# Optimization experiments

Hardware: AMD Instinct MI355X
Metric: run time of the kernel (lower is better)

The kernel has to match this reference:

```python
import jax, jax.numpy as jnp
import numpy as np

N, D, E, T = 30000, 256, 300000, 2
HID, OUT, HEADS = 64, 256, 8


def setup_inputs() -> dict:
    key = jax.random.key(0)
    ks = jax.random.split(key, 16)
    g = lambda k, shape, fan_in: jax.random.normal(k, shape, jnp.float32) / np.sqrt(fan_in)
    inp = {
        'x': jax.random.normal(ks[0], (N, D), jnp.float32),
        'edge_index': jax.random.randint(ks[1], (T, 2, E), 0, N, jnp.int32),
        'w1_l': g(ks[2], (T, D, HEADS * HID), D),
        'b1_l': jnp.zeros((T, HEADS * HID), jnp.float32),
        'w1_r': g(ks[3], (T, D, HEADS * HID), D),
        'b1_r': jnp.zeros((T, HEADS * HID), jnp.float32),
        'att1': g(ks[4], (T, HEADS, HID), HID),
        'bias1': jnp.zeros((T, HEADS * HID), jnp.float32),
        'w2_l': g(ks[5], (T, HEADS * HID, OUT), HEADS * HID),
        'b2_l': jnp.zeros((T, OUT), jnp.float32),
        'w2_r': g(ks[6], (T, HEADS * HID, OUT), HEADS * HID),
        'b2_r': jnp.zeros((T, OUT), jnp.float32),
        'att2': g(ks[7], (T, 1, OUT), OUT),
        'bias2': jnp.zeros((T, OUT), jnp.float32),
        'w_lin': g(ks[8], (OUT, OUT), OUT),
        'b_lin': jnp.zeros((OUT,), jnp.float32),
    }
    return inp


def _gatv2(x, src, dst, w_l, b_l, w_r, b_r, att, bias, num_nodes):
    # GATv2Conv: e = att . leaky_relu(W_l x_src + W_r x_dst); softmax over in-edges of dst;
    # out = scatter_add(alpha * W_l x_src) per destination; concat heads + bias.
    H, C = att.shape
    xl = (x @ w_l + b_l).reshape(num_nodes, H, C)
    xr = (x @ w_r + b_r).reshape(num_nodes, H, C)
    h = jax.nn.leaky_relu(xl[src] + xr[dst], 0.2)      # [E, H, C]
    e = jnp.einsum('ehc,hc->eh', h, att)               # [E, H]
    m = jax.ops.segment_max(e, dst, num_segments=num_nodes)
    p = jnp.exp(e - m[dst])
    s = jax.ops.segment_sum(p, dst, num_segments=num_nodes)
    alpha = p / s[dst]                                 # softmax over neighbors
    out = jax.ops.segment_sum(xl[src] * alpha[:, :, None], dst, num_segments=num_nodes)
    return out.reshape(num_nodes, H * C) + bias


def reference(x, edge_index, w1_l, b1_l, w1_r, b1_r, att1, bias1,
              w2_l, b2_l, w2_r, b2_r, att2, bias2, w_lin, b_lin):
    n = x.shape[0]
    loop = jnp.arange(n, dtype=edge_index.dtype)  # GATv2Conv default add_self_loops=True
    srcs, dsts = [], []
    for t in range(edge_index.shape[0]):
        srcs.append(jnp.concatenate([edge_index[t, 0], loop]))
        dsts.append(jnp.concatenate([edge_index[t, 1], loop]))

    # conv1 (heads=8, concat) with HeteroConv aggr='sum'
    h1 = jnp.zeros((n, w1_l.shape[2]), x.dtype)
    for t in range(len(srcs)):
        h1 = h1 + _gatv2(x, srcs[t], dsts[t], w1_l[t], b1_l[t], w1_r[t], b1_r[t], att1[t], bias1[t], n)
    h1 = jax.nn.elu(h1)

    # conv2 (heads=1, concat=False -> mean over 1 head == identity)
    h2 = jnp.zeros((n, w2_l.shape[2]), x.dtype)
    for t in range(len(srcs)):
        h2 = h2 + _gatv2(h1, srcs[t], dsts[t], w2_l[t], b2_l[t], w2_r[t], b2_r[t], att2[t], bias2[t], n)
    h2 = jax.nn.elu(h2)

    return h2 @ w_lin + b_lin
```

## Files before the change

kernel.cpp:

```cpp
#include <hip/hip_runtime.h>
#include <math.h>

#define N_NODES 30000
#define D_IN    256
#define E_EDGES 300000
#define T_TYPES 2
#define HEADS   8
#define HID     64
#define F1      512
#define OUT_F   256
#define EP      (E_EDGES + N_NODES)

typedef __attribute__((ext_vector_type(8))) short bf16x8;
typedef __attribute__((ext_vector_type(4))) float f32x4;

__device__ __forceinline__ unsigned short f2bf(float f) {
    unsigned u = __float_as_uint(f);
    unsigned r = 0x7fffu + ((u >> 16) & 1u);
    return (unsigned short)((u + r) >> 16);
}
__device__ __forceinline__ float bf2f(unsigned short h) {
    return __uint_as_float(((unsigned)h) << 16);
}

__device__ __forceinline__ void gload16(const void* g, void* l) {
    __builtin_amdgcn_global_load_lds(
        (const __attribute__((address_space(1))) unsigned int*)g,
        (__attribute__((address_space(3))) unsigned int*)l, 16, 0, 0);
}

#define PREP_W1   (8 * 65536)
#define PREP_W2   (4 * 131072)
#define PREP_WL   65536
#define PREP_CNT  (T_TYPES * N_NODES)
#define PREP_TOT  (PREP_W1 + PREP_W2 + PREP_WL + PREP_CNT)

__global__ void prep_kernel(const float* __restrict__ w1_l, const float* __restrict__ w1_r,
                            const float* __restrict__ w2_l, const float* __restrict__ w2_r,
                            const float* __restrict__ w_lin,
                            unsigned short* __restrict__ wt1h, unsigned short* __restrict__ wt1l,
                            unsigned short* __restrict__ wt2h, unsigned short* __restrict__ wt2l,
                            unsigned short* __restrict__ wtLh, unsigned short* __restrict__ wtLl,
                            int* __restrict__ count) {
    int idx = blockIdx.x * blockDim.x + threadIdx.x;
    if (idx < PREP_W1) {
        int n = idx & 255, k = (idx >> 8) & 255, mat = idx >> 16;
        int h = mat & 1, lr = (mat >> 1) & 1, t = mat >> 2;
        const float* src = lr ? w1_r : w1_l;
        float v = src[(size_t)t * 256 * 512 + (size_t)k * 512 + h * 256 + n];
        unsigned short hi = f2bf(v);
        unsigned short lo = f2bf(v - bf2f(hi));
        size_t o = (size_t)mat * 65536 + (size_t)n * 256 + k;
        wt1h[o] = hi; wt1l[o] = lo;
        return;
    }
    idx -= PREP_W1;
    if (idx < PREP_W2) {
        int n = idx & 255, k = (idx >> 8) & 511, mat = idx >> 17;
        int lr = mat & 1, t = mat >> 1;
        const float* src = lr ? w2_r : w2_l;
        float v = src[(size_t)t * 512 * 256 + (size_t)k * 256 + n];
        unsigned short hi = f2bf(v);
        unsigned short lo = f2bf(v - bf2f(hi));
        size_t o = (size_t)mat * 131072 + (size_t)n * 512 + k;
        wt2h[o] = hi; wt2l[o] = lo;
        return;
    }
    idx -= PREP_W2;
    if (idx < PREP_WL) {
        int n = idx & 255, k = idx >> 8;
        float v = w_lin[k * 256 + n];
        unsigned short hi = f2bf(v);
        unsigned short lo = f2bf(v - bf2f(hi));
        size_t o = (size_t)n * 256 + k;
        wtLh[o] = hi; wtLl[o] = lo;
        return;
    }
    idx -= PREP_WL;
    if (idx < PREP_CNT) count[idx] = 0;
}

__global__ void hist_kernel(const int* __restrict__ ei, int* __restrict__ count) {
    int idx = blockIdx.x * blockDim.x + threadIdx.x;
    if (idx >= T_TYPES * EP) return;
    int t = idx / EP, i = idx - t * EP;
    int dst = (i < E_EDGES) ? ei[t * 2 * E_EDGES + E_EDGES + i] : (i - E_EDGES);
    atomicAdd(&count[t * N_NODES + dst], 1);
}

#define SCAN_NB 30

__global__ __launch_bounds__(256) void scan_bsum_kernel(const int* __restrict__ cnt,
                                                        int* __restrict__ bsum) {
    int t = blockIdx.y, b = blockIdx.x;
    const int* c = cnt + t * N_NODES;
    int i0 = b * 1024 + threadIdx.x * 4;
    int s = 0;
    #pragma unroll
    for (int j = 0; j < 4; ++j) { int i = i0 + j; if (i < N_NODES) s += c[i]; }
    #pragma unroll
    for (int m = 1; m < 64; m <<= 1) s += __shfl_xor(s, m);
    __shared__ int wsum[4];
    int l = threadIdx.x & 63, w = threadIdx.x >> 6;
    if (l == 0) wsum[w] = s;
    __syncthreads();
    if (threadIdx.x == 0) bsum[t * SCAN_NB + b] = wsum[0] + wsum[1] + wsum[2] + wsum[3];
}

__global__ void scan_base_kernel(int* __restrict__ bsum) {
    int t = threadIdx.x;
    if (t >= T_TYPES) return;
    int acc = 0;
    for (int b = 0; b < SCAN_NB; ++b) {
        int v = bsum[t * SCAN_NB + b];
        bsum[t * SCAN_NB + b] = acc;
        acc += v;
    }
}

__global__ __launch_bounds__(256) void scan_write_kernel(int* __restrict__ cnt,
                                                         const int* __restrict__ bsum,
                                                         int* __restrict__ off) {
    int t = blockIdx.y, b = blockIdx.x;
    int tid = threadIdx.x;
    int* c = cnt + t * N_NODES;
    int* o = off + t * (N_NODES + 1);
    int i0 = b * 1024 + tid * 4;
    int v[4]; int s = 0;
    #pragma unroll
    for (int j = 0; j < 4; ++j) { int i = i0 + j; v[j] = (i < N_NODES) ? c[i] : 0; s += v[j]; }
    __shared__ int ps[256];
    ps[tid] = s;
    __syncthreads();
    for (int ofs = 1; ofs < 256; ofs <<= 1) {
        int x = (tid >= ofs) ? ps[tid - ofs] : 0;
        __syncthreads();
        ps[tid] += x;
        __syncthreads();
    }
    int base = bsum[t * SCAN_NB + b] + ps[tid] - s;
    #pragma unroll
    for (int j = 0; j < 4; ++j) {
        int i = i0 + j;
        if (i < N_NODES) { o[i] = base; base += v[j]; c[i] = 0; }
    }
    if (b == 0 && tid == 0) o[N_NODES] = EP;
}

__global__ void scatter_kernel(const int* __restrict__ ei, const int* __restrict__ offsets,
                               int* __restrict__ cursor, int* __restrict__ csr_src) {
    int idx = blockIdx.x * blockDim.x + threadIdx.x;
    if (idx >= T_TYPES * EP) return;
    int t = idx / EP, i = idx - t * EP;
    int src, dst;
    if (i < E_EDGES) {
        src = ei[t * 2 * E_EDGES + i];
        dst = ei[t * 2 * E_EDGES + E_EDGES + i];
    } else {
        src = dst = i - E_EDGES;
    }
    int pos = offsets[t * (N_NODES + 1) + dst] + atomicAdd(&cursor[t * N_NODES + dst], 1);
    csr_src[t * EP + pos] = src;
}

template <int ASPLIT>
__global__ __launch_bounds__(256) void gemm_mfma_kernel(
        const void* __restrict__ A0v, const void* __restrict__ A1v, int lda,
        const unsigned short* __restrict__ Bh0, const unsigned short* __restrict__ Bl0,
        const float* __restrict__ bias0, float* __restrict__ C0,
        const unsigned short* __restrict__ Bh1, const unsigned short* __restrict__ Bl1,
        const float* __restrict__ bias1, float* __restrict__ C1,
        int M, int K) {
    const unsigned short* Bh = blockIdx.y ? Bh1 : Bh0;
    const unsigned short* Bl = blockIdx.y ? Bl1 : Bl0;
    const float* bias = blockIdx.y ? bias1 : bias0;
    float* C = blockIdx.y ? C1 : C0;
    const float* Af          = (const float*)A0v;
    const unsigned short* Ah = (const unsigned short*)A0v;
    const unsigned short* Al = (const unsigned short*)A1v;

    __shared__ unsigned short Ah_s[64 * 32], Al_s[64 * 32];
    __shared__ unsigned short Bh_s[256 * 32], Bl_s[256 * 32];
    int t = threadIdx.x;
    int row0 = blockIdx.x * 64;
    int w = t >> 6;
    int l = t & 63;
    int fm = l & 15;
    int fg = l >> 4;

    f32x4 acc[4][4];
    const f32x4 zf = {0.f, 0.f, 0.f, 0.f};
    #pragma unroll
    for (int i = 0; i < 4; ++i)
        #pragma unroll
        for (int j = 0; j < 4; ++j) acc[i][j] = zf;

    int ar = t >> 3, af = t & 7;
    int rs = l >> 2, cs = l & 3;

    for (int k0 = 0; k0 < K; k0 += 32) {
        #pragma unroll
        for (int g = 0; g < 4; ++g) {
            int n = g * 64 + w * 16 + rs;
            int swn = (n >> 1) & 3;
            size_t so = (size_t)n * K + k0 + ((cs ^ swn) * 8);
            gload16(&Bh[so], &Bh_s[(g * 64 + w * 16) * 32]);
            gload16(&Bl[so], &Bl_s[(g * 64 + w * 16) * 32]);
        }
        if constexpr (ASPLIT == 0) {
            #pragma unroll
            for (int v = 0; v < 2; ++v) {
                int r = v * 32 + ar;
                int rg = row0 + r;
                float4 a4 = make_float4(0.f, 0.f, 0.f, 0.f);
                if (rg < M) a4 = *(const float4*)&Af[(size_t)rg * lda + k0 + af * 4];
                ushort4 hi, lo;
                hi.x = f2bf(a4.x); lo.x = f2bf(a4.x - bf2f(hi.x));
                hi.y = f2bf(a4.y); lo.y = f2bf(a4.y - bf2f(hi.y));
                hi.z = f2bf(a4.z); lo.z = f2bf(a4.z - bf2f(hi.z));
                hi.w = f2bf(a4.w); lo.w = f2bf(a4.w - bf2f(hi.w));
                int ke = (af * 4) ^ (((r >> 1) & 3) << 3);
                *(ushort4*)&Ah_s[r * 32 + ke] = hi;
                *(ushort4*)&Al_s[r * 32 + ke] = lo;
            }
        } else {
            int r = w * 16 + rs;
            int rg = row0 + r;
            if (rg >= M) rg = M - 1;
            int swn = (r >> 1) & 3;
            size_t so = (size_t)rg * lda + k0 + ((cs ^ swn) * 8);
            gload16(&Ah[so], &Ah_s[(w * 16) * 32]);
            gload16(&Al[so], &Al_s[(w * 16) * 32]);
        }
        __syncthreads();
        bf16x8 ahf[4], alf[4], bhf[4], blf[4];
        #pragma unroll
        for (int i = 0; i < 4; ++i) {
            int r = i * 16 + fm;
            int ke = (fg * 8) ^ (((r >> 1) & 3) << 3);
            ahf[i] = *(const bf16x8*)&Ah_s[r * 32 + ke];
            alf[i] = *(const bf16x8*)&Al_s[r * 32 + ke];
        }
        #pragma unroll
        for (int j = 0; j < 4; ++j) {
            int n = w * 64 + j * 16 + fm;
            int ke = (fg * 8) ^ (((n >> 1) & 3) << 3);
            bhf[j] = *(const bf16x8*)&Bh_s[n * 32 + ke];
            blf[j] = *(const bf16x8*)&Bl_s[n * 32 + ke];
        }
        #pragma unroll
        for (int i = 0; i < 4; ++i)
            #pragma unroll
            for (int j = 0; j < 4; ++j) {
                acc[i][j] = __builtin_amdgcn_mfma_f32_16x16x32_bf16(ahf[i], bhf[j], acc[i][j], 0, 0, 0);
                acc[i][j] = __builtin_amdgcn_mfma_f32_16x16x32_bf16(ahf[i], blf[j], acc[i][j], 0, 0, 0);
                acc[i][j] = __builtin_amdgcn_mfma_f32_16x16x32_bf16(alf[i], bhf[j], acc[i][j], 0, 0, 0);
            }
        __syncthreads();
    }
    #pragma unroll
    for (int j = 0; j < 4; ++j) {
        int col = w * 64 + j * 16 + fm;
        float bv = bias[col];
        #pragma unroll
        for (int i = 0; i < 4; ++i) {
            #pragma unroll
            for (int q = 0; q < 4; ++q) {
                int rg = row0 + i * 16 + fg * 4 + q;
                if (rg < M) C[(size_t)rg * 256 + col] = acc[i][j][q] + bv;
            }
        }
    }
}

template <int RW, int MODE>
__global__ __launch_bounds__(256) void gat_edge_kernel(
        const float* __restrict__ xl, const float* __restrict__ xr,
        const float* __restrict__ att,
        const int* __restrict__ offs, const int* __restrict__ csr,
        float* __restrict__ out, int ldo,
        const float* __restrict__ eb0, const float* __restrict__ eb1,
        unsigned short* __restrict__ sh, unsigned short* __restrict__ sl) {
    int wave = (blockIdx.x * blockDim.x + threadIdx.x) >> 6;
    int lane = threadIdx.x & 63;
    if (wave >= N_NODES) return;
    int d = wave;
    int q4 = lane * 4;
    float attr[4], xrr[4];
    *(float4*)&attr[0] = *(const float4*)&att[q4];
    *(float4*)&xrr[0]  = *(const float4*)&xr[(size_t)d * 256 + q4];
    float m = -INFINITY, s = 0.f;
    float acc[4] = {0.f, 0.f, 0.f, 0.f};
    int p0 = offs[d], p1 = offs[d + 1];
    int p = p0;
    for (; p + 2 <= p1; p += 2) {
        int s0 = csr[p], s1 = csr[p + 1];
        float xv0[4], xv1[4];
        *(float4*)&xv0[0] = *(const float4*)&xl[(size_t)s0 * 256 + q4];
        *(float4*)&xv1[0] = *(const float4*)&xl[(size_t)s1 * 256 + q4];
        float e0 = 0.f, e1 = 0.f;
        #pragma unroll
        for (int q = 0; q < 4; ++q) {
            float h0 = xv0[q] + xrr[q];
            float h1 = xv1[q] + xrr[q];
            h0 = (h0 > 0.f) ? h0 : 0.2f * h0;
            h1 = (h1 > 0.f) ? h1 : 0.2f * h1;
            e0 += attr[q] * h0;
            e1 += attr[q] * h1;
        }
        #pragma unroll
        for (int msk = 1; msk < RW; msk <<= 1) {
            e0 += __shfl_xor(e0, msk);
            e1 += __shfl_xor(e1, msk);
        }
        float mn = fmaxf(m, e0);
        float sc = __expf(m - mn);
        float pe = __expf(e0 - mn);
        s = s * sc + pe;
        #pragma unroll
        for (int q = 0; q < 4; ++q) acc[q] = acc[q] * sc + pe * xv0[q];
        m = mn;
        mn = fmaxf(m, e1);
        sc = __expf(m - mn);
        pe = __expf(e1 - mn);
        s = s * sc + pe;
        #pragma unroll
        for (int q = 0; q < 4; ++q) acc[q] = acc[q] * sc + pe * xv1[q];
        m = mn;
    }
    if (p < p1) {
        int s0 = csr[p];
        float xv0[4];
        *(float4*)&xv0[0] = *(const float4*)&xl[(size_t)s0 * 256 + q4];
        float e0 = 0.f;
        #pragma unroll
        for (int q = 0; q < 4; ++q) {
            float h0 = xv0[q] + xrr[q];
            h0 = (h0 > 0.f) ? h0 : 0.2f * h0;
            e0 += attr[q] * h0;
        }
        #pragma unroll
        for (int msk = 1; msk < RW; msk <<= 1) e0 += __shfl_xor(e0, msk);
        float mn = fmaxf(m, e0);
        float sc = __expf(m - mn);
        float pe = __expf(e0 - mn);
        s = s * sc + pe;
        #pragma unroll
        for (int q = 0; q < 4; ++q) acc[q] = acc[q] * sc + pe * xv0[q];
        m = mn;
    }
    float inv = 1.f / s;
    float* dp = &out[(size_t)d * ldo + q4];
    if (MODE == 0) {
        *(float4*)dp = make_float4(acc[0] * inv, acc[1] * inv, acc[2] * inv, acc[3] * inv);
    } else if (MODE == 2) {
        #pragma unroll
        for (int q = 0; q < 4; ++q) {
            float v = dp[q] + acc[q] * inv + eb0[q4 + q] + eb1[q4 + q];
            dp[q] = (v > 0.f) ? v : (__expf(v) - 1.f);
        }
    } else {
        ushort4 hv, lv;
        float v0 = dp[0] + acc[0] * inv + eb0[q4 + 0] + eb1[q4 + 0];
        float v1 = dp[1] + acc[1] * inv + eb0[q4 + 1] + eb1[q4 + 1];
        float v2 = dp[2] + acc[2] * inv + eb0[q4 + 2] + eb1[q4 + 2];
        float v3 = dp[3] + acc[3] * inv + eb0[q4 + 3] + eb1[q4 + 3];
        v0 = (v0 > 0.f) ? v0 : (__expf(v0) - 1.f);
        v1 = (v1 > 0.f) ? v1 : (__expf(v1) - 1.f);
        v2 = (v2 > 0.f) ? v2 : (__expf(v2) - 1.f);
        v3 = (v3 > 0.f) ? v3 : (__expf(v3) - 1.f);
        hv.x = f2bf(v0); lv.x = f2bf(v0 - bf2f(hv.x));
        hv.y = f2bf(v1); lv.y = f2bf(v1 - bf2f(hv.y));
        hv.z = f2bf(v2); lv.z = f2bf(v2 - bf2f(hv.z));
        hv.w = f2bf(v3); lv.w = f2bf(v3 - bf2f(hv.w));
        *(ushort4*)&sh[(size_t)d * ldo + q4] = hv;
        *(ushort4*)&sl[(size_t)d * ldo + q4] = lv;
    }
}

extern "C" void kernel_launch(void* const* d_in, const int* in_sizes, int n_in,
                              void* d_out, int out_size, void* d_ws, size_t ws_size,
                              hipStream_t stream) {
    const float* x      = (const float*)d_in[0];
    const int*   ei     = (const int*)d_in[1];
    const float* w1_l   = (const float*)d_in[2];
    const float* b1_l   = (const float*)d_in[3];
    const float* w1_r   = (const float*)d_in[4];
    const float* b1_r   = (const float*)d_in[5];
    const float* att1   = (const float*)d_in[6];
    const float* bias1  = (const float*)d_in[7];
    const float* w2_l   = (const float*)d_in[8];
    const float* b2_l   = (const float*)d_in[9];
    const float* w2_r   = (const float*)d_in[10];
    const float* b2_r   = (const float*)d_in[11];
    const float* att2   = (const float*)d_in[12];
    const float* bias2  = (const float*)d_in[13];
    const float* w_lin  = (const float*)d_in[14];
    const float* b_lin  = (const float*)d_in[15];
    float* out = (float*)d_out;

    float* h1   = (float*)d_ws;
    float* bufA = h1 + (size_t)N_NODES * F1;
    float* bufB = bufA + (size_t)N_NODES * OUT_F;
    unsigned short* wt1h = (unsigned short*)(bufB + (size_t)N_NODES * OUT_F);
    unsigned short* wt1l = wt1h + 8 * 65536;
    unsigned short* wt2h = wt1l + 8 * 65536;
    unsigned short* wt2l = wt2h + 4 * 131072;
    unsigned short* wtLh = wt2l + 4 * 131072;
    unsigned short* wtLl = wtLh + 65536;
    int* count   = (int*)(wtLl + 65536);
    int* offsets = count + T_TYPES * N_NODES;
    int* bsum    = offsets + T_TYPES * (N_NODES + 1);
    int* csr     = bsum + T_TYPES * SCAN_NB;
    unsigned short* h2s_hi = (unsigned short*)h1;
    unsigned short* h2s_lo = h2s_hi + (size_t)N_NODES * OUT_F;

    prep_kernel<<<(PREP_TOT + 255) / 256, 256, 0, stream>>>(
        w1_l, w1_r, w2_l, w2_r, w_lin, wt1h, wt1l, wt2h, wt2l, wtLh, wtLl, count);

    int eblocks = (T_TYPES * EP + 255) / 256;
    hist_kernel<<<eblocks, 256, 0, stream>>>(ei, count);
    dim3 sgrid(SCAN_NB, T_TYPES);
    scan_bsum_kernel<<<sgrid, 256, 0, stream>>>(count, bsum);
    scan_base_kernel<<<1, 64, 0, stream>>>(bsum);
    scan_write_kernel<<<sgrid, 256, 0, stream>>>(count, bsum, offsets);
    scatter_kernel<<<eblocks, 256, 0, stream>>>(ei, offsets, count, csr);

    int gat_blocks = N_NODES / 4;
    dim3 ggrid((N_NODES + 63) / 64, 2);
    dim3 ggrid1((N_NODES + 63) / 64, 1);

    for (int t = 0; t < T_TYPES; ++t) {
        for (int hh = 0; hh < 2; ++hh) {
            int co = hh * 256;
            int ml = (t * 2 + 0) * 2 + hh, mr = (t * 2 + 1) * 2 + hh;
            gemm_mfma_kernel<0><<<ggrid, 256, 0, stream>>>(
                x, nullptr, D_IN,
                wt1h + (size_t)ml * 65536, wt1l + (size_t)ml * 65536, b1_l + t * F1 + co, bufA,
                wt1h + (size_t)mr * 65536, wt1l + (size_t)mr * 65536, b1_r + t * F1 + co, bufB,
                N_NODES, D_IN);
            if (t == 0)
                gat_edge_kernel<16, 0><<<gat_blocks, 256, 0, stream>>>(
                    bufA, bufB, att1 + t * F1 + co, offsets + t * (N_NODES + 1),
                    csr + (size_t)t * EP, h1 + co, F1, nullptr, nullptr, nullptr, nullptr);
            else
                gat_edge_kernel<16, 2><<<gat_blocks, 256, 0, stream>>>(
                    bufA, bufB, att1 + t * F1 + co, offsets + t * (N_NODES + 1),
                    csr + (size_t)t * EP, h1 + co, F1, bias1 + co, bias1 + F1 + co,
                    nullptr, nullptr);
        }
    }

    for (int t = 0; t < T_TYPES; ++t) {
        int ml = t * 2 + 0, mr = t * 2 + 1;
        gemm_mfma_kernel<0><<<ggrid, 256, 0, stream>>>(
            h1, nullptr, F1,
            wt2h + (size_t)ml * 131072, wt2l + (size_t)ml * 131072, b2_l + t * OUT_F, bufA,
            wt2h + (size_t)mr * 131072, wt2l + (size_t)mr * 131072, b2_r + t * OUT_F, bufB,
            N_NODES, F1);
        if (t == 0)
            gat_edge_kernel<64, 0><<<gat_blocks, 256, 0, stream>>>(
                bufA, bufB, att2 + t * OUT_F, offsets + t * (N_NODES + 1),
                csr + (size_t)t * EP, out, OUT_F, nullptr, nullptr, nullptr, nullptr);
        else
            gat_edge_kernel<64, 3><<<gat_blocks, 256, 0, stream>>>(
                bufA, bufB, att2 + t * OUT_F, offsets + t * (N_NODES + 1),
                csr + (size_t)t * EP, out, OUT_F, bias2, bias2 + OUT_F,
                h2s_hi, h2s_lo);
    }

    gemm_mfma_kernel<1><<<ggrid1, 256, 0, stream>>>(
        h2s_hi, h2s_lo, OUT_F,
        wtLh, wtLl, b_lin, out,
        wtLh, wtLl, b_lin, out,
        N_NODES, OUT_F);
}
```

Before: 892.3 us.

## Double-buffer shared-memory tiles in split-bf16 MFMA GEMM to overlap loads with compute

Shared-memory A and B tiles in the GEMM kernel are now double-buffered. The next K-slice is staged (async global-to-LDS loads for B and pre-split A, register prefetch for fp32 A) while MFMAs run on the current slice, so each iteration needs one barrier instead of two. The goal is to hide global load latency behind the matrix math. It doubles LDS use to about 80KB per block, which may cut occupancy, and fp32 A is held in registers one extra stage ahead.

```diff
diff --git a/kernel.cpp b/kernel.cpp
--- a/kernel.cpp
+++ b/kernel.cpp
@@ -163,6 +163,60 @@
     csr_src[t * EP + pos] = src;
 }
 
+#define STAGE_B(BUF, K0)                                                     \
+    do {                                                                     \
+        _Pragma("unroll")                                                    \
+        for (int g = 0; g < 4; ++g) {                                        \
+            int n_ = g * 64 + w * 16 + rs;                                   \
+            int swn_ = (n_ >> 1) & 3;                                        \
+            size_t so_ = (size_t)n_ * K + (K0) + ((cs ^ swn_) * 8);          \
+            gload16(&Bh[so_], &Bh_s[BUF][(g * 64 + w * 16) * 32]);           \
+            gload16(&Bl[so_], &Bl_s[BUF][(g * 64 + w * 16) * 32]);           \
+        }                                                                    \
+    } while (0)
+
+#define STAGE_A_DMA(BUF, K0)                                                 \
+    do {                                                                     \
+        int r_ = w * 16 + rs;                                                \
+        int rg_ = row0 + r_;                                                 \
+        if (rg_ >= M) rg_ = M - 1;                                           \
+        int swn_ = (r_ >> 1) & 3;                                            \
+        size_t so_ = (size_t)rg_ * lda + (K0) + ((cs ^ swn_) * 8);           \
+        gload16(&Ah[so_], &Ah_s[BUF][(w * 16) * 32]);                        \
+        gload16(&Al[so_], &Al_s[BUF][(w * 16) * 32]);                        \
+    } while (0)
+
+#define LOAD_A_REGS(K0)                                                      \
+    do {                                                                     \
+        int rg0_ = row0 + ar;                                                \
+        int rg1_ = row0 + 32 + ar;                                           \
+        aN0 = (rg0_ < M) ? *(const float4*)&Af[(size_t)rg0_ * lda + (K0) + af * 4] \
+                         : make_float4(0.f, 0.f, 0.f, 0.f);                  \
+        aN1 = (rg1_ < M) ? *(const float4*)&Af[(size_t)rg1_ * lda + (K0) + af * 4] \
+                         : make_float4(0.f, 0.f, 0.f, 0.f);                  \
+    } while (0)
+
+#define WRITE_A(BUF)                                                         \
+    do {                                                                     \
+        ushort4 hi_, lo_;                                                    \
+        int r_ = ar;                                                         \
+        hi_.x = f2bf(aN0.x); lo_.x = f2bf(aN0.x - bf2f(hi_.x));              \
+        hi_.y = f2bf(aN0.y); lo_.y = f2bf(aN0.y - bf2f(hi_.y));              \
+        hi_.z = f2bf(aN0.z); lo_.z = f2bf(aN0.z - bf2f(hi_.z));              \
+        hi_.w = f2bf(aN0.w); lo_.w = f2bf(aN0.w - bf2f(hi_.w));              \
+        int ke_ = (af * 4) ^ (((r_ >> 1) & 3) << 3);                         \
+        *(ushort4*)&Ah_s[BUF][r_ * 32 + ke_] = hi_;                          \
+        *(ushort4*)&Al_s[BUF][r_ * 32 + ke_] = lo_;                          \
+        r_ = 32 + ar;                                                        \
+        hi_.x = f2bf(aN1.x); lo_.x = f2bf(aN1.x - bf2f(hi_.x));              \
+        hi_.y = f2bf(aN1.y); lo_.y = f2bf(aN1.y - bf2f(hi_.y));              \
+        hi_.z = f2bf(aN1.z); lo_.z = f2bf(aN1.z - bf2f(hi_.z));              \
+        hi_.w = f2bf(aN1.w); lo_.w = f2bf(aN1.w - bf2f(hi_.w));              \
+        ke_ = (af * 4) ^ (((r_ >> 1) & 3) << 3);                             \
+        *(ushort4*)&Ah_s[BUF][r_ * 32 + ke_] = hi_;                          \
+        *(ushort4*)&Al_s[BUF][r_ * 32 + ke_] = lo_;                          \
+    } while (0)
+
 template <int ASPLIT>
 __global__ __launch_bounds__(256) void gemm_mfma_kernel(
         const void* __restrict__ A0v, const void* __restrict__ A1v, int lda,
@@ -179,8 +233,8 @@
     const unsigned short* Ah = (const unsigned short*)A0v;
     const unsigned short* Al = (const unsigned short*)A1v;
 
-    __shared__ unsigned short Ah_s[64 * 32], Al_s[64 * 32];
-    __shared__ unsigned short Bh_s[256 * 32], Bl_s[256 * 32];
+    __shared__ unsigned short Ah_s[2][64 * 32], Al_s[2][64 * 32];
+    __shared__ unsigned short Bh_s[2][256 * 32], Bl_s[2][256 * 32];
     int t = threadIdx.x;
     int row0 = blockIdx.x * 64;
     int w = t >> 6;
@@ -198,63 +252,54 @@
     int ar = t >> 3, af = t & 7;
     int rs = l >> 2, cs = l & 3;
 
-    for (int k0 = 0; k0 < K; k0 += 32) {
-        #pragma unroll
-        for (int g = 0; g < 4; ++g) {
-            int n = g * 64 + w * 16 + rs;
-            int swn = (n >> 1) & 3;
-            size_t so = (size_t)n * K + k0 + ((cs ^ swn) * 8);
-            gload16(&Bh[so], &Bh_s[(g * 64 + w * 16) * 32]);
-            gload16(&Bl[so], &Bl_s[(g * 64 + w * 16) * 32]);
-        }
-        if constexpr (ASPLIT == 0) {
-            #pragma unroll
-            for (int v = 0; v < 2; ++v) {
-                int r = v * 32 + ar;
-                int rg = row0 + r;
-                float4 a4 = make_float4(0.f, 0.f, 0.f, 0.f);
-                if (rg < M) a4 = *(const float4*)&Af[(size_t)rg * lda + k0 + af * 4];
-                ushort4 hi, lo;
-                hi.x = f2bf(a4.x); lo.x = f2bf(a4.x - bf2f(hi.x));
-                hi.y = f2bf(a4.y); lo.y = f2bf(a4.y - bf2f(hi.y));
-                hi.z = f2bf(a4.z); lo.z = f2bf(a4.z - bf2f(hi.z));
-                hi.w = f2bf(a4.w); lo.w = f2bf(a4.w - bf2f(hi.w));
-                int ke = (af * 4) ^ (((r >> 1) & 3) << 3);
-                *(ushort4*)&Ah_s[r * 32 + ke] = hi;
-                *(ushort4*)&Al_s[r * 32 + ke] = lo;
+    float4 aN0, aN1;
+    int nk = K >> 5;
+
+    if constexpr (ASPLIT == 0) {
+        LOAD_A_REGS(0);
+        STAGE_B(0, 0);
+        WRITE_A(0);
+        if (nk > 1) LOAD_A_REGS(32);
+    } else {
+        STAGE_B(0, 0);
+        STAGE_A_DMA(0, 0);
+    }
+    __syncthreads();
+
+    for (int i = 0; i < nk; ++i) {
+        int cur = i & 1, nxt = cur ^ 1;
+        if (i + 1 < nk) {
+            int k1 = (i + 1) << 5;
+            STAGE_B(nxt, k1);
+            if constexpr (ASPLIT == 0) {
+                WRITE_A(nxt);
+                if (i + 2 < nk) LOAD_A_REGS(k1 + 32);
+            } else {
+                STAGE_A_DMA(nxt, k1);
             }
-        } else {
-            int r = w * 16 + rs;
-            int rg = row0 + r;
-            if (rg >= M) rg = M - 1;
-            int swn = (r >> 1) & 3;
-            size_t so = (size_t)rg * lda + k0 + ((cs ^ swn) * 8);
-            gload16(&Ah[so], &Ah_s[(w * 16) * 32]);
-            gload16(&Al[so], &Al_s[(w * 16) * 32]);
-        }
-        __syncthreads();
+        }
         bf16x8 ahf[4], alf[4], bhf[4], blf[4];
         #pragma unroll
-        for (int i = 0; i < 4; ++i) {
-            int r = i * 16 + fm;
+        for (int ii = 0; ii < 4; ++ii) {
+            int r = ii * 16 + fm;
             int ke = (fg * 8) ^ (((r >> 1) & 3) << 3);
-            ahf[i] = *(const bf16x8*)&Ah_s[r * 32 + ke];
-            alf[i] = *(const bf16x8*)&Al_s[r * 32 + ke];
+            ahf[ii] = *(const bf16x8*)&Ah_s[cur][r * 32 + ke];
+            alf[ii] = *(const bf16x8*)&Al_s[cur][r * 32 + ke];
         }
         #pragma unroll
         for (int j = 0; j < 4; ++j) {
             int n = w * 64 + j * 16 + fm;
             int ke = (fg * 8) ^ (((n >> 1) & 3) << 3);
-            bhf[j] = *(const bf16x8*)&Bh_s[n * 32 + ke];
-            blf[j] = *(const bf16x8*)&Bl_s[n * 32 + ke];
-        }
-        #pragma unroll
-        for (int i = 0; i < 4; ++i)
+            bhf[j] = *(const bf16x8*)&Bh_s[cur][n * 32 + ke];
+            blf[j] = *(const bf16x8*)&Bl_s[cur][n * 32 + ke];
+        }
+        #pragma unroll
+        for (int ii = 0; ii < 4; ++ii)
             #pragma unroll
             for (int j = 0; j < 4; ++j) {
-                acc[i][j] = __builtin_amdgcn_mfma_f32_16x16x32_bf16(ahf[i], bhf[j], acc[i][j], 0, 0, 0);
-                acc[i][j] = __builtin_amdgcn_mfma_f32_16x16x32_bf16(ahf[i], blf[j], acc[i][j], 0, 0, 0);
-                acc[i][j] = __builtin_amdgcn_mfma_f32_16x16x32_bf16(alf[i], bhf[j], acc[i][j], 0, 0, 0);
+                acc[ii][j] = __builtin_amdgcn_mfma_f32_16x16x32_bf16(ahf[ii], bhf[j], acc[ii][j], 0, 0, 0);
+                acc[ii][j] = __builtin_amdgcn_mfma_f32_16x16x32_bf16(ahf[ii], blf[j], acc[ii][j], 0, 0, 0);
+                acc[ii][j] = __builtin_amdgcn_mfma_f32_16x16x32_bf16(alf[ii], bhf[j], acc[ii][j], 0, 0, 0);
             }
         __syncthreads();
     }
```

Result: faster. 862.8 us (-3.3%).
